# Performance work log

Hardware: AMD Instinct MI355X
Metric: run time of the kernel (lower is better)

Reference implementation:

```python
import jax, jax.numpy as jnp
import numpy as np

D = 64          # embed_dim == latent dim
T = 200         # diffusion_steps, timestep_respacing='' -> full 200 reverse steps
B, L = 8192, 100
N_ITEMS = 100000


def setup_inputs() -> dict:
    key = jax.random.key(0)
    ks = jax.random.split(key, 16)

    def lin(k, i, o):
        return (jax.random.normal(k, (i, o), jnp.float32) / np.sqrt(i)).astype(jnp.float32)

    item_seq = jax.random.randint(ks[0], (B, L), 0, N_ITEMS)
    item_emb = jax.random.normal(ks[1], (N_ITEMS, D), jnp.float32) * 0.02
    item_emb = item_emb.at[0].set(0.0)  # padding_idx=0
    return {
        'item_seq': item_seq,
        'item_emb': item_emb,
        'W_enc1': lin(ks[2], D, 256), 'b_enc1': jnp.zeros((256,), jnp.float32),
        'W_enc2': lin(ks[3], 256, 2 * D), 'b_enc2': jnp.zeros((2 * D,), jnp.float32),
        'W_in': lin(ks[4], D, D), 'b_in': jnp.zeros((D,), jnp.float32),
        'W_t': lin(ks[5], D, D), 'b_t': jnp.zeros((D,), jnp.float32),
        'W_c': lin(ks[6], D, D), 'b_c': jnp.zeros((D,), jnp.float32),
        'W_out': lin(ks[7], D, D), 'b_out': jnp.zeros((D,), jnp.float32),
    }


def _schedule():
    # improved-diffusion linear schedule
    scale = 1000.0 / T
    betas = jnp.linspace(scale * 1e-4, scale * 0.02, T, dtype=jnp.float32)
    alphas = 1.0 - betas
    acp = jnp.cumprod(alphas)
    acp_prev = jnp.concatenate([jnp.ones((1,), jnp.float32), acp[:-1]])
    sqrt_recip = jnp.sqrt(1.0 / acp)
    sqrt_recipm1 = jnp.sqrt(1.0 / acp - 1.0)
    post_var = betas * (1.0 - acp_prev) / (1.0 - acp)
    post_logvar = jnp.log(jnp.concatenate([post_var[1:2], post_var[1:]]))  # clipped
    coef1 = betas * jnp.sqrt(acp_prev) / (1.0 - acp)
    coef2 = (1.0 - acp_prev) * jnp.sqrt(alphas) / (1.0 - acp)
    return sqrt_recip, sqrt_recipm1, post_logvar, coef1, coef2


def reference(item_seq, item_emb, W_enc1, b_enc1, W_enc2, b_enc2,
              W_in, b_in, W_t, b_t, W_c, b_c, W_out, b_out):
    # ---- pooled VAE encoder (eval mode: dropout = identity, z = mu) ----
    seq = item_emb[item_seq]                                   # [B, L, D] gather
    cnt = jnp.sum(item_seq != 0, axis=1, keepdims=True).astype(seq.dtype)
    pooled = jnp.sum(seq, axis=1) / jnp.sqrt(cnt)              # [B, D]
    h = jax.nn.relu(pooled @ W_enc1 + b_enc1)
    enc = h @ W_enc2 + b_enc2                                  # [B, 2D]
    mu, logvar = jnp.split(enc, 2, axis=-1)
    z = mu                                                     # eval reparameterize

    # ---- ScoreNet: eps-prediction MLP conditioned on x_start and sinusoidal t ----
    half = D // 2
    freqs = jnp.exp(-jnp.log(10000.0) * jnp.arange(half, dtype=jnp.float32) / half)

    def scorenet(x, t_float, cond):
        ang = t_float * freqs                                  # [D/2]
        temb = jnp.concatenate([jnp.cos(ang), jnp.sin(ang)])   # [D]
        hh = jax.nn.silu(x @ W_in + b_in + (temb @ W_t + b_t) + cond @ W_c + b_c)
        return hh @ W_out + b_out                              # eps, [B, D]

    # ---- p_sample_loop (FIXED_SMALL variance, clip_denoised=True) ----
    sqrt_recip, sqrt_recipm1, post_logvar, coef1, coef2 = _schedule()
    x_init = jax.random.normal(jax.random.key(1), z.shape, z.dtype)
    noise_key = jax.random.key(2)

    def step(x, t):
        eps = scorenet(x, t.astype(jnp.float32), z)
        x0 = jnp.clip(sqrt_recip[t] * x - sqrt_recipm1[t] * eps, -1.0, 1.0)
        mean = coef1[t] * x0 + coef2[t] * x
        noise = jax.random.normal(jax.random.fold_in(noise_key, t), x.shape, x.dtype)
        sigma = jnp.where(t > 0, jnp.exp(0.5 * post_logvar[t]), 0.0)
        return mean + sigma * noise, None

    sample, _ = jax.lax.scan(step, x_init, jnp.arange(T - 1, -1, -1))
    return sample
```

## Files before the change

### kernel.cpp

```cpp
#include <hip/hip_runtime.h>
#include <cstdint>


#define DEVI __device__ __forceinline__

typedef __attribute__((ext_vector_type(8))) short short8;
typedef __attribute__((ext_vector_type(4))) float f32x4;

DEVI void threefry2x32(uint32_t k0, uint32_t k1, uint32_t x0, uint32_t x1,
                       uint32_t &o0, uint32_t &o1)
{
  const uint32_t ks2 = k0 ^ k1 ^ 0x1BD11BDAu;
  x0 += k0; x1 += k1;
#define TFR(r) { x0 += x1; x1 = __builtin_rotateleft32(x1, r); x1 ^= x0; }
  TFR(13u) TFR(15u) TFR(26u) TFR(6u)   x0 += k1;  x1 += ks2 + 1u;
  TFR(17u) TFR(29u) TFR(16u) TFR(24u)  x0 += ks2; x1 += k0 + 2u;
  TFR(13u) TFR(15u) TFR(26u) TFR(6u)   x0 += k0;  x1 += k1 + 3u;
  TFR(17u) TFR(29u) TFR(16u) TFR(24u)  x0 += k1;  x1 += ks2 + 4u;
  TFR(13u) TFR(15u) TFR(26u) TFR(6u)   x0 += ks2; x1 += k0 + 5u;
#undef TFR
  o0 = x0; o1 = x1;
}

DEVI uint32_t jax_random_bits32(uint32_t k0, uint32_t k1, uint32_t j)
{
  uint32_t a, b;
  threefry2x32(k0, k1, 0u, j, a, b);
  return a ^ b;
}

DEVI float jax_bits_to_normal(uint32_t bits)
{
  const float LO = -0.99999994f;
  float f = __uint_as_float((bits >> 9) | 0x3f800000u) - 1.0f;
  float u = fmaxf(LO, f * 2.0f + LO);
  float w = -__logf((1.0f - u) * (1.0f + u));
  float p;
  if (w < 5.0f) {
    w = w - 2.5f;
    p =              2.81022636e-08f;
    p = fmaf(p, w,   3.43273939e-07f);
    p = fmaf(p, w,  -3.5233877e-06f);
    p = fmaf(p, w,  -4.39150654e-06f);
    p = fmaf(p, w,   0.00021858087f);
    p = fmaf(p, w,  -0.00125372503f);
    p = fmaf(p, w,  -0.00417768164f);
    p = fmaf(p, w,   0.246640727f);
    p = fmaf(p, w,   1.50140941f);
  } else {
    w = sqrtf(w) - 3.0f;
    p =             -0.000200214257f;
    p = fmaf(p, w,   0.000100950558f);
    p = fmaf(p, w,   0.00134934322f);
    p = fmaf(p, w,  -0.00367342844f);
    p = fmaf(p, w,   0.00573950773f);
    p = fmaf(p, w,  -0.0076224613f);
    p = fmaf(p, w,   0.00943887047f);
    p = fmaf(p, w,   1.00167406f);
    p = fmaf(p, w,   2.83297682f);
  }
  return 1.41421356237f * (p * u);
}

DEVI short bf16_hi_trunc(float x) { return (short)(__float_as_uint(x) >> 16); }
DEVI float bf16_to_f32(short h)
{
  return __uint_as_float(((uint32_t)(unsigned short)h) << 16);
}
DEVI void split_bf16(float x, short &h, short &l)
{
  h = bf16_hi_trunc(x);
  float r = x - bf16_to_f32(h);
  l = bf16_hi_trunc(r);
}

DEVI short8 ld_frag16(const short* p)
{
  union { int4 v; short8 s; } u;
  u.v = *(const int4*)p;
  return u.s;
}

__global__ __launch_bounds__(256)
void k_pool(const int* __restrict__ seq, const float* __restrict__ emb,
            float* __restrict__ pooled)
{
  const int lane = threadIdx.x & 63;
  const int r    = blockIdx.x * 4 + (threadIdx.x >> 6);
  const int* row = seq + r * 100;
  float s = 0.f;
  int cnt = 0;
  for (int l = 0; l < 100; ++l) {
    int id = row[l];
    cnt += (id != 0);
    s += emb[id * 64 + lane];
  }
  pooled[r * 64 + lane] = s / sqrtf((float)cnt);
}

__global__ __launch_bounds__(256)
void k_enc(const float* __restrict__ pooled,
           const float* __restrict__ W1, const float* __restrict__ b1,
           const float* __restrict__ W2, const float* __restrict__ b2,
           const float* __restrict__ Wc, const float* __restrict__ bc,
           float* __restrict__ cproj)
{
  __shared__ float p_s[8][64];
  __shared__ float h_s[8][256];
  __shared__ float mu_s[8][64];
  const int tid = threadIdx.x;
  const int r0  = blockIdx.x * 8;

  for (int i = tid; i < 8 * 64; i += 256)
    p_s[i >> 6][i & 63] = pooled[r0 * 64 + i];
  __syncthreads();

  float hacc[8];
#pragma unroll
  for (int r = 0; r < 8; ++r) hacc[r] = b1[tid];
  for (int k = 0; k < 64; ++k) {
    float w = W1[k * 256 + tid];
#pragma unroll
    for (int r = 0; r < 8; ++r) hacc[r] = fmaf(p_s[r][k], w, hacc[r]);
  }
#pragma unroll
  for (int r = 0; r < 8; ++r) h_s[r][tid] = fmaxf(hacc[r], 0.f);
  __syncthreads();

#pragma unroll
  for (int pass = 0; pass < 2; ++pass) {
    int r = pass * 4 + (tid >> 6);
    int j = tid & 63;
    float acc = b2[j];
    for (int k = 0; k < 256; ++k)
      acc = fmaf(h_s[r][k], W2[k * 128 + j], acc);
    mu_s[r][j] = acc;
  }
  __syncthreads();

#pragma unroll
  for (int pass = 0; pass < 2; ++pass) {
    int r = pass * 4 + (tid >> 6);
    int j = tid & 63;
    float acc = bc[j];
    for (int k = 0; k < 64; ++k)
      acc = fmaf(mu_s[r][k], Wc[k * 64 + j], acc);
    cproj[(r0 + r) * 64 + j] = acc;
  }
}

__global__ __launch_bounds__(64)
void k_prep(const float* __restrict__ Wt, const float* __restrict__ bt,
            const float* __restrict__ bin, float* __restrict__ tpb,
            float* __restrict__ sched)
{
  __shared__ float temb[64];
  const int t = blockIdx.x;
  const int d = threadIdx.x;
  const float lg = logf(10000.0f);
  {
    int i = d & 31;
    float fr  = expf((-lg * (float)i) / 32.0f);
    float ang = (float)t * fr;
    temb[d] = (d < 32) ? cosf(ang) : sinf(ang);
  }
  if (d == 0) {
    const float start = (float)(5.0 * 1e-4);
    const float stop  = (float)(5.0 * 0.02);
    const float delta = stop - start;
    float prod = 1.f, acp_prev = 1.f, beta = 0.f, alpha = 1.f;
    for (int i = 0; i <= t; ++i) {
      beta  = start + ((float)i * delta) / 199.0f;
      alpha = 1.0f - beta;
      acp_prev = prod;
      prod = prod * alpha;
    }
    float acp = prod;
    float om  = 1.0f - acp;
    sched[t * 8 + 0] = sqrtf(1.0f / acp);
    sched[t * 8 + 1] = sqrtf(1.0f / acp - 1.0f);
    sched[t * 8 + 2] = beta * sqrtf(acp_prev) / om;
    sched[t * 8 + 3] = (1.0f - acp_prev) * sqrtf(alpha) / om;
    float pv = beta * (1.0f - acp_prev) / om;
    sched[t * 8 + 4] = (t > 0) ? sqrtf(pv) : 0.0f;
    uint32_t fk0, fk1;
    threefry2x32(0u, 2u, 0u, (uint32_t)t, fk0, fk1);
    ((uint32_t*)sched)[t * 8 + 5] = fk0;
    ((uint32_t*)sched)[t * 8 + 6] = fk1;
  }
  __syncthreads();
  float acc = bt[d] + bin[d];
  for (int k = 0; k < 64; ++k)
    acc = fmaf(temb[k], Wt[k * 64 + d], acc);
  tpb[t * 64 + d] = acc;
}

#define XLDW  72

__global__
__attribute__((amdgpu_flat_work_group_size(512, 512), amdgpu_waves_per_eu(4, 4)))
void k_ddpm(const float* __restrict__ Win, const float* __restrict__ Wout,
            const float* __restrict__ bout,
            const float* __restrict__ cproj, const float* __restrict__ tpb,
            const float* __restrict__ sched, float* __restrict__ out)
{
  __shared__ __align__(16) short Xh[16 * XLDW], Xl[16 * XLDW];
  __shared__ __align__(16) short Hh[16 * XLDW], Hl[16 * XLDW];

  const int tid  = threadIdx.x;
  const int lane = tid & 63;
  const int w    = tid >> 6;
  const int nt   = w & 3;
  const int kc   = w >> 2;
  const int nn   = lane & 15;
  const int quad = lane >> 4;
  const int dim  = nt * 16 + nn;
  const int arow = nn;
  const int r0g  = blockIdx.x * 16;
  const int kq0  = quad * 8;
  const int kq1  = 32 + quad * 8;
  const int rA   = quad * 4 + 2 * kc;

  short8 wiH0, wiL0, wiH1, wiL1, woH0, woL0, woH1, woL1;
#pragma unroll
  for (int j = 0; j < 8; ++j) {
    short h, l;
    split_bf16(Win[(kq0 + j) * 64 + dim], h, l);  wiH0[j] = h; wiL0[j] = l;
    split_bf16(Win[(kq1 + j) * 64 + dim], h, l);  wiH1[j] = h; wiL1[j] = l;
    split_bf16(Wout[(kq0 + j) * 64 + dim], h, l); woH0[j] = h; woL0[j] = l;
    split_bf16(Wout[(kq1 + j) * 64 + dim], h, l); woH1[j] = h; woL1[j] = l;
  }

  const float bo = bout[dim];
  const uint32_t jA = (uint32_t)((r0g + rA) * 64 + dim);
  const uint32_t jB = jA + 64u;
  const float cpA = cproj[jA];
  const float cpB = cproj[jB];

  float xoA = jax_bits_to_normal(jax_random_bits32(0u, 1u, jA));
  float xoB = jax_bits_to_normal(jax_random_bits32(0u, 1u, jB));
  {
    short h, l;
    split_bf16(xoA, h, l); Xh[rA * XLDW + dim] = h; Xl[rA * XLDW + dim] = l;
    split_bf16(xoB, h, l); Xh[(rA+1) * XLDW + dim] = h; Xl[(rA+1) * XLDW + dim] = l;
  }
  __syncthreads();

  float tp = tpb[199 * 64 + dim];

#pragma unroll 1
  for (int t = 199; t >= 0; --t) {
    const float sr   = sched[t * 8 + 0];
    const float srm1 = sched[t * 8 + 1];
    const float c1   = sched[t * 8 + 2];
    const float c2   = sched[t * 8 + 3];
    const float sg   = sched[t * 8 + 4];
    const uint32_t fk0 = ((const uint32_t*)sched)[t * 8 + 5];
    const uint32_t fk1 = ((const uint32_t*)sched)[t * 8 + 6];

    float nA = jax_bits_to_normal(jax_random_bits32(fk0, fk1, jA));
    float nB = jax_bits_to_normal(jax_random_bits32(fk0, fk1, jB));

    f32x4 acc;
    if (kc == 0) { acc[0] = tp + cpA; acc[1] = tp + cpB; acc[2] = 0.f; acc[3] = 0.f; }
    else         { acc[0] = 0.f; acc[1] = 0.f; acc[2] = tp + cpA; acc[3] = tp + cpB; }
    {
      short8 xh0 = ld_frag16(&Xh[arow * XLDW + kq0]);
      short8 xl0 = ld_frag16(&Xl[arow * XLDW + kq0]);
      short8 xh1 = ld_frag16(&Xh[arow * XLDW + kq1]);
      short8 xl1 = ld_frag16(&Xl[arow * XLDW + kq1]);
      acc = __builtin_amdgcn_mfma_f32_16x16x32_bf16(xl0, wiH0, acc, 0, 0, 0);
      acc = __builtin_amdgcn_mfma_f32_16x16x32_bf16(xh0, wiL0, acc, 0, 0, 0);
      acc = __builtin_amdgcn_mfma_f32_16x16x32_bf16(xh0, wiH0, acc, 0, 0, 0);
      acc = __builtin_amdgcn_mfma_f32_16x16x32_bf16(xl1, wiH1, acc, 0, 0, 0);
      acc = __builtin_amdgcn_mfma_f32_16x16x32_bf16(xh1, wiL1, acc, 0, 0, 0);
      acc = __builtin_amdgcn_mfma_f32_16x16x32_bf16(xh1, wiH1, acc, 0, 0, 0);
    }
    {
      float vA, vB;
      if (kc == 0) { vA = acc[0]; vB = acc[1]; }
      else         { vA = acc[2]; vB = acc[3]; }
      vA = vA * __builtin_amdgcn_rcpf(1.0f + __expf(-vA));
      vB = vB * __builtin_amdgcn_rcpf(1.0f + __expf(-vB));
      short h, l;
      split_bf16(vA, h, l); Hh[rA * XLDW + dim] = h; Hl[rA * XLDW + dim] = l;
      split_bf16(vB, h, l); Hh[(rA+1) * XLDW + dim] = h; Hl[(rA+1) * XLDW + dim] = l;
    }
    int tn = (t > 0) ? (t - 1) : 0;
    float tpn = tpb[tn * 64 + dim];
    __syncthreads();

    f32x4 eac;
    if (kc == 0) { eac[0] = bo; eac[1] = bo; eac[2] = 0.f; eac[3] = 0.f; }
    else         { eac[0] = 0.f; eac[1] = 0.f; eac[2] = bo; eac[3] = bo; }
    {
      short8 hh0 = ld_frag16(&Hh[arow * XLDW + kq0]);
      short8 hl0 = ld_frag16(&Hl[arow * XLDW + kq0]);
      short8 hh1 = ld_frag16(&Hh[arow * XLDW + kq1]);
      short8 hl1 = ld_frag16(&Hl[arow * XLDW + kq1]);
      eac = __builtin_amdgcn_mfma_f32_16x16x32_bf16(hl0, woH0, eac, 0, 0, 0);
      eac = __builtin_amdgcn_mfma_f32_16x16x32_bf16(hh0, woL0, eac, 0, 0, 0);
      eac = __builtin_amdgcn_mfma_f32_16x16x32_bf16(hh0, woH0, eac, 0, 0, 0);
      eac = __builtin_amdgcn_mfma_f32_16x16x32_bf16(hl1, woH1, eac, 0, 0, 0);
      eac = __builtin_amdgcn_mfma_f32_16x16x32_bf16(hh1, woL1, eac, 0, 0, 0);
      eac = __builtin_amdgcn_mfma_f32_16x16x32_bf16(hh1, woH1, eac, 0, 0, 0);
    }
    {
      float eA, eB;
      if (kc == 0) { eA = eac[0]; eB = eac[1]; }
      else         { eA = eac[2]; eB = eac[3]; }
      float xcA = fminf(1.f, fmaxf(-1.f, sr * xoA - srm1 * eA));
      float xcB = fminf(1.f, fmaxf(-1.f, sr * xoB - srm1 * eB));
      xoA = c1 * xcA + c2 * xoA + sg * nA;
      xoB = c1 * xcB + c2 * xoB + sg * nB;
      short h, l;
      split_bf16(xoA, h, l); Xh[rA * XLDW + dim] = h; Xl[rA * XLDW + dim] = l;
      split_bf16(xoB, h, l); Xh[(rA+1) * XLDW + dim] = h; Xl[(rA+1) * XLDW + dim] = l;
      tp = tpn;
    }
    __syncthreads();
  }

  out[jA] = xoA;
  out[jB] = xoB;
}

extern "C" void kernel_launch(void* const* d_in, const int* in_sizes, int n_in,
                              void* d_out, int out_size, void* d_ws, size_t ws_size,
                              hipStream_t stream)
{
  const int*   seq  = (const int*)  d_in[0];
  const float* emb  = (const float*)d_in[1];
  const float* W1   = (const float*)d_in[2];
  const float* b1   = (const float*)d_in[3];
  const float* W2   = (const float*)d_in[4];
  const float* b2   = (const float*)d_in[5];
  const float* Win  = (const float*)d_in[6];
  const float* bin  = (const float*)d_in[7];
  const float* Wt   = (const float*)d_in[8];
  const float* bt   = (const float*)d_in[9];
  const float* Wc   = (const float*)d_in[10];
  const float* bc   = (const float*)d_in[11];
  const float* Wout = (const float*)d_in[12];
  const float* bout = (const float*)d_in[13];

  float* out   = (float*)d_out;
  float* ws    = (float*)d_ws;
  float* cproj = ws;
  float* tpb   = ws + 524288;
  float* sched = ws + 524288 + 12800;
  float* pooled = out;

  k_pool <<<2048, 256, 0, stream>>>(seq, emb, pooled);
  k_enc  <<<1024, 256, 0, stream>>>(pooled, W1, b1, W2, b2, Wc, bc, cproj);
  k_prep <<<200, 64, 0, stream>>>(Wt, bt, bin, tpb, sched);
  k_ddpm <<<512, 512, 0, stream>>>(Win, Wout, bout, cproj, tpb, sched, out);
}
```

Baseline: 561.4 us.

## Precompute all diffusion noise in a parallel kernel before the sampling loop

Adds a k_noise kernel that generates the threefry-based Gaussian noise for all 200 timesteps into a large workspace buffer. The serial k_ddpm loop then loads each step's noise from memory instead of computing the RNG inline. This takes the integer hash work off the latency-bound sequential loop and runs it in a fully parallel launch. In exchange it writes and later reads about 400 MB of noise. It is only enabled when the workspace is large enough, otherwise the old inline path is used.

```diff
diff --git a/kernel.cpp b/kernel.cpp
--- a/kernel.cpp
+++ b/kernel.cpp
@@ -195,14 +195,32 @@
   tpb[t * 64 + d] = acc;
 }
 
+__global__ __launch_bounds__(256)
+void k_noise(const float* __restrict__ sched, float* __restrict__ noise)
+{
+  const uint32_t base = (blockIdx.x * 256u + threadIdx.x) * 4u;
+  const uint32_t t = base >> 19;
+  const uint32_t j = base & 524287u;
+  const uint32_t fk0 = ((const uint32_t*)sched)[t * 8 + 5];
+  const uint32_t fk1 = ((const uint32_t*)sched)[t * 8 + 6];
+  float4 v;
+  v.x = jax_bits_to_normal(jax_random_bits32(fk0, fk1, j + 0u));
+  v.y = jax_bits_to_normal(jax_random_bits32(fk0, fk1, j + 1u));
+  v.z = jax_bits_to_normal(jax_random_bits32(fk0, fk1, j + 2u));
+  v.w = jax_bits_to_normal(jax_random_bits32(fk0, fk1, j + 3u));
+  *(float4*)(noise + base) = v;
+}
+
 #define XLDW  72
 
+template <bool PRE>
 __global__
 __attribute__((amdgpu_flat_work_group_size(512, 512), amdgpu_waves_per_eu(4, 4)))
 void k_ddpm(const float* __restrict__ Win, const float* __restrict__ Wout,
             const float* __restrict__ bout,
             const float* __restrict__ cproj, const float* __restrict__ tpb,
-            const float* __restrict__ sched, float* __restrict__ out)
+            const float* __restrict__ sched, const float* __restrict__ noise,
+            float* __restrict__ out)
 {
   __shared__ __align__(16) short Xh[16 * XLDW], Xl[16 * XLDW];
   __shared__ __align__(16) short Hh[16 * XLDW], Hl[16 * XLDW];
@@ -255,11 +273,18 @@
     const float c1   = sched[t * 8 + 2];
     const float c2   = sched[t * 8 + 3];
     const float sg   = sched[t * 8 + 4];
-    const uint32_t fk0 = ((const uint32_t*)sched)[t * 8 + 5];
-    const uint32_t fk1 = ((const uint32_t*)sched)[t * 8 + 6];
-
-    float nA = jax_bits_to_normal(jax_random_bits32(fk0, fk1, jA));
-    float nB = jax_bits_to_normal(jax_random_bits32(fk0, fk1, jB));
+
+    float nA, nB;
+    if (PRE) {
+      const float* np = noise + (uint32_t)t * 524288u;
+      nA = np[jA];
+      nB = np[jB];
+    } else {
+      const uint32_t fk0 = ((const uint32_t*)sched)[t * 8 + 5];
+      const uint32_t fk1 = ((const uint32_t*)sched)[t * 8 + 6];
+      nA = jax_bits_to_normal(jax_random_bits32(fk0, fk1, jA));
+      nB = jax_bits_to_normal(jax_random_bits32(fk0, fk1, jB));
+    }
 
     f32x4 acc;
     if (kc == 0) { acc[0] = tp + cpA; acc[1] = tp + cpB; acc[2] = 0.f; acc[3] = 0.f; }
@@ -349,10 +374,18 @@
   float* cproj = ws;
   float* tpb   = ws + 524288;
   float* sched = ws + 524288 + 12800;
+  float* noise = ws + 538688;
   float* pooled = out;
+
+  const bool pre = ws_size >= (538688ull + 104857600ull) * 4ull;
 
   k_pool <<<2048, 256, 0, stream>>>(seq, emb, pooled);
   k_enc  <<<1024, 256, 0, stream>>>(pooled, W1, b1, W2, b2, Wc, bc, cproj);
   k_prep <<<200, 64, 0, stream>>>(Wt, bt, bin, tpb, sched);
-  k_ddpm <<<512, 512, 0, stream>>>(Win, Wout, bout, cproj, tpb, sched, out);
-}
+  if (pre) {
+    k_noise<<<102400, 256, 0, stream>>>(sched, noise);
+    k_ddpm<true> <<<512, 512, 0, stream>>>(Win, Wout, bout, cproj, tpb, sched, noise, out);
+  } else {
+    k_ddpm<false><<<512, 512, 0, stream>>>(Win, Wout, bout, cproj, tpb, sched, noise, out);
+  }
+}
```

New measurement: 562.4 us. No clear change (+0.2%).

## Specialize warps: four do GEMV steps, four pre-generate next-step noise

Applied to the files above, without the earlier changes.

Splits the 8 waves of each block into two roles. Four waves do the two MFMA GEMVs and the update for all 16 rows, each covering all four accumulator rows. The other four waves compute next-step threefry normal noise into a double-buffered shared-memory buffer. This takes the RNG cost off the critical path of the sequential diffusion loop, but it removes the old split-K duplication, so the GEMV waves now do four rows each and half the waves are producers.

```diff
diff --git a/kernel.cpp b/kernel.cpp
--- a/kernel.cpp
+++ b/kernel.cpp
@@ -196,6 +196,7 @@
 }
 
 #define XLDW  72
+#define NBW   68
 
 __global__
 __attribute__((amdgpu_flat_work_group_size(512, 512), amdgpu_waves_per_eu(4, 4)))
@@ -206,123 +207,155 @@
 {
   __shared__ __align__(16) short Xh[16 * XLDW], Xl[16 * XLDW];
   __shared__ __align__(16) short Hh[16 * XLDW], Hl[16 * XLDW];
+  __shared__ __align__(16) float nbuf[2 * 16 * NBW];
 
   const int tid  = threadIdx.x;
   const int lane = tid & 63;
   const int w    = tid >> 6;
+  const bool gemv = (w < 4);
+  const int r0g  = blockIdx.x * 16;
+  const uint32_t* su = (const uint32_t*)sched;
+
   const int nt   = w & 3;
-  const int kc   = w >> 2;
   const int nn   = lane & 15;
   const int quad = lane >> 4;
   const int dim  = nt * 16 + nn;
   const int arow = nn;
-  const int r0g  = blockIdx.x * 16;
   const int kq0  = quad * 8;
   const int kq1  = 32 + quad * 8;
-  const int rA   = quad * 4 + 2 * kc;
+  const int rowb = quad * 4;
+
+  const int q    = (w - 4) * 64 + lane;
+  const int cb   = q * 4;
+  const uint32_t jn = (uint32_t)(r0g * 64 + cb);
+  const int nrow = cb >> 6;
+  const int ndim = cb & 63;
+  float* nb_w = &nbuf[nrow * NBW + ndim];
 
   short8 wiH0, wiL0, wiH1, wiL1, woH0, woL0, woH1, woL1;
-#pragma unroll
-  for (int j = 0; j < 8; ++j) {
-    short h, l;
-    split_bf16(Win[(kq0 + j) * 64 + dim], h, l);  wiH0[j] = h; wiL0[j] = l;
-    split_bf16(Win[(kq1 + j) * 64 + dim], h, l);  wiH1[j] = h; wiL1[j] = l;
-    split_bf16(Wout[(kq0 + j) * 64 + dim], h, l); woH0[j] = h; woL0[j] = l;
-    split_bf16(Wout[(kq1 + j) * 64 + dim], h, l); woH1[j] = h; woL1[j] = l;
-  }
-
-  const float bo = bout[dim];
-  const uint32_t jA = (uint32_t)((r0g + rA) * 64 + dim);
-  const uint32_t jB = jA + 64u;
-  const float cpA = cproj[jA];
-  const float cpB = cproj[jB];
-
-  float xoA = jax_bits_to_normal(jax_random_bits32(0u, 1u, jA));
-  float xoB = jax_bits_to_normal(jax_random_bits32(0u, 1u, jB));
-  {
-    short h, l;
-    split_bf16(xoA, h, l); Xh[rA * XLDW + dim] = h; Xl[rA * XLDW + dim] = l;
-    split_bf16(xoB, h, l); Xh[(rA+1) * XLDW + dim] = h; Xl[(rA+1) * XLDW + dim] = l;
-  }
-  __syncthreads();
-
-  float tp = tpb[199 * 64 + dim];
+  float cp[4], xo[4];
+  float bo = 0.f, tp = 0.f;
+  uint32_t j0 = 0;
+
+  if (gemv) {
+#pragma unroll
+    for (int j = 0; j < 8; ++j) {
+      short h, l;
+      split_bf16(Win[(kq0 + j) * 64 + dim], h, l);  wiH0[j] = h; wiL0[j] = l;
+      split_bf16(Win[(kq1 + j) * 64 + dim], h, l);  wiH1[j] = h; wiL1[j] = l;
+      split_bf16(Wout[(kq0 + j) * 64 + dim], h, l); woH0[j] = h; woL0[j] = l;
+      split_bf16(Wout[(kq1 + j) * 64 + dim], h, l); woH1[j] = h; woL1[j] = l;
+    }
+    bo = bout[dim];
+    j0 = (uint32_t)((r0g + rowb) * 64 + dim);
+#pragma unroll
+    for (int r = 0; r < 4; ++r) cp[r] = cproj[j0 + r * 64u];
+#pragma unroll
+    for (int r = 0; r < 4; ++r) {
+      xo[r] = jax_bits_to_normal(jax_random_bits32(0u, 1u, j0 + r * 64u));
+      short h, l;
+      split_bf16(xo[r], h, l);
+      Xh[(rowb + r) * XLDW + dim] = h; Xl[(rowb + r) * XLDW + dim] = l;
+    }
+    tp = tpb[199 * 64 + dim];
+  } else {
+    const uint32_t fk0 = su[199 * 8 + 5];
+    const uint32_t fk1 = su[199 * 8 + 6];
+    float* d = nb_w + 16 * NBW;
+    d[0] = jax_bits_to_normal(jax_random_bits32(fk0, fk1, jn + 0u));
+    d[1] = jax_bits_to_normal(jax_random_bits32(fk0, fk1, jn + 1u));
+    d[2] = jax_bits_to_normal(jax_random_bits32(fk0, fk1, jn + 2u));
+    d[3] = jax_bits_to_normal(jax_random_bits32(fk0, fk1, jn + 3u));
+  }
+  __syncthreads();
 
 #pragma unroll 1
   for (int t = 199; t >= 0; --t) {
-    const float sr   = sched[t * 8 + 0];
-    const float srm1 = sched[t * 8 + 1];
-    const float c1   = sched[t * 8 + 2];
-    const float c2   = sched[t * 8 + 3];
-    const float sg   = sched[t * 8 + 4];
-    const uint32_t fk0 = ((const uint32_t*)sched)[t * 8 + 5];
-    const uint32_t fk1 = ((const uint32_t*)sched)[t * 8 + 6];
-
-    float nA = jax_bits_to_normal(jax_random_bits32(fk0, fk1, jA));
-    float nB = jax_bits_to_normal(jax_random_bits32(fk0, fk1, jB));
-
+    float sr = 0.f, srm1 = 0.f, c1 = 0.f, c2 = 0.f, sg = 0.f;
+    float n[4], tpn = 0.f;
     f32x4 acc;
-    if (kc == 0) { acc[0] = tp + cpA; acc[1] = tp + cpB; acc[2] = 0.f; acc[3] = 0.f; }
-    else         { acc[0] = 0.f; acc[1] = 0.f; acc[2] = tp + cpA; acc[3] = tp + cpB; }
-    {
-      short8 xh0 = ld_frag16(&Xh[arow * XLDW + kq0]);
-      short8 xl0 = ld_frag16(&Xl[arow * XLDW + kq0]);
-      short8 xh1 = ld_frag16(&Xh[arow * XLDW + kq1]);
-      short8 xl1 = ld_frag16(&Xl[arow * XLDW + kq1]);
-      acc = __builtin_amdgcn_mfma_f32_16x16x32_bf16(xl0, wiH0, acc, 0, 0, 0);
-      acc = __builtin_amdgcn_mfma_f32_16x16x32_bf16(xh0, wiL0, acc, 0, 0, 0);
-      acc = __builtin_amdgcn_mfma_f32_16x16x32_bf16(xh0, wiH0, acc, 0, 0, 0);
-      acc = __builtin_amdgcn_mfma_f32_16x16x32_bf16(xl1, wiH1, acc, 0, 0, 0);
-      acc = __builtin_amdgcn_mfma_f32_16x16x32_bf16(xh1, wiL1, acc, 0, 0, 0);
-      acc = __builtin_amdgcn_mfma_f32_16x16x32_bf16(xh1, wiH1, acc, 0, 0, 0);
-    }
-    {
-      float vA, vB;
-      if (kc == 0) { vA = acc[0]; vB = acc[1]; }
-      else         { vA = acc[2]; vB = acc[3]; }
-      vA = vA * __builtin_amdgcn_rcpf(1.0f + __expf(-vA));
-      vB = vB * __builtin_amdgcn_rcpf(1.0f + __expf(-vB));
-      short h, l;
-      split_bf16(vA, h, l); Hh[rA * XLDW + dim] = h; Hl[rA * XLDW + dim] = l;
-      split_bf16(vB, h, l); Hh[(rA+1) * XLDW + dim] = h; Hl[(rA+1) * XLDW + dim] = l;
-    }
-    int tn = (t > 0) ? (t - 1) : 0;
-    float tpn = tpb[tn * 64 + dim];
+    uint32_t gk0 = 0, gk1 = 0;
+    float* nd = nullptr;
+
+    if (gemv) {
+      sr   = sched[t * 8 + 0];
+      srm1 = sched[t * 8 + 1];
+      c1   = sched[t * 8 + 2];
+      c2   = sched[t * 8 + 3];
+      sg   = sched[t * 8 + 4];
+      const float* nr = &nbuf[(t & 1) * 16 * NBW + rowb * NBW + dim];
+#pragma unroll
+      for (int r = 0; r < 4; ++r) n[r] = nr[r * NBW];
+
+#pragma unroll
+      for (int r = 0; r < 4; ++r) acc[r] = tp + cp[r];
+      {
+        short8 xh0 = ld_frag16(&Xh[arow * XLDW + kq0]);
+        short8 xl0 = ld_frag16(&Xl[arow * XLDW + kq0]);
+        short8 xh1 = ld_frag16(&Xh[arow * XLDW + kq1]);
+        short8 xl1 = ld_frag16(&Xl[arow * XLDW + kq1]);
+        acc = __builtin_amdgcn_mfma_f32_16x16x32_bf16(xl0, wiH0, acc, 0, 0, 0);
+        acc = __builtin_amdgcn_mfma_f32_16x16x32_bf16(xh0, wiL0, acc, 0, 0, 0);
+        acc = __builtin_amdgcn_mfma_f32_16x16x32_bf16(xh0, wiH0, acc, 0, 0, 0);
+        acc = __builtin_amdgcn_mfma_f32_16x16x32_bf16(xl1, wiH1, acc, 0, 0, 0);
+        acc = __builtin_amdgcn_mfma_f32_16x16x32_bf16(xh1, wiL1, acc, 0, 0, 0);
+        acc = __builtin_amdgcn_mfma_f32_16x16x32_bf16(xh1, wiH1, acc, 0, 0, 0);
+      }
+#pragma unroll
+      for (int r = 0; r < 4; ++r) {
+        float v = acc[r];
+        v = v * __builtin_amdgcn_rcpf(1.0f + __expf(-v));
+        short h, l;
+        split_bf16(v, h, l);
+        Hh[(rowb + r) * XLDW + dim] = h; Hl[(rowb + r) * XLDW + dim] = l;
+      }
+      int tn = (t > 0) ? (t - 1) : 0;
+      tpn = tpb[tn * 64 + dim];
+    } else if (t > 0) {
+      gk0 = su[(t - 1) * 8 + 5];
+      gk1 = su[(t - 1) * 8 + 6];
+      nd = nb_w + ((t - 1) & 1) * 16 * NBW;
+      nd[0] = jax_bits_to_normal(jax_random_bits32(gk0, gk1, jn + 0u));
+      nd[1] = jax_bits_to_normal(jax_random_bits32(gk0, gk1, jn + 1u));
+    }
     __syncthreads();
 
-    f32x4 eac;
-    if (kc == 0) { eac[0] = bo; eac[1] = bo; eac[2] = 0.f; eac[3] = 0.f; }
-    else         { eac[0] = 0.f; eac[1] = 0.f; eac[2] = bo; eac[3] = bo; }
-    {
-      short8 hh0 = ld_frag16(&Hh[arow * XLDW + kq0]);
-      short8 hl0 = ld_frag16(&Hl[arow * XLDW + kq0]);
-      short8 hh1 = ld_frag16(&Hh[arow * XLDW + kq1]);
-      short8 hl1 = ld_frag16(&Hl[arow * XLDW + kq1]);
-      eac = __builtin_amdgcn_mfma_f32_16x16x32_bf16(hl0, woH0, eac, 0, 0, 0);
-      eac = __builtin_amdgcn_mfma_f32_16x16x32_bf16(hh0, woL0, eac, 0, 0, 0);
-      eac = __builtin_amdgcn_mfma_f32_16x16x32_bf16(hh0, woH0, eac, 0, 0, 0);
-      eac = __builtin_amdgcn_mfma_f32_16x16x32_bf16(hl1, woH1, eac, 0, 0, 0);
-      eac = __builtin_amdgcn_mfma_f32_16x16x32_bf16(hh1, woL1, eac, 0, 0, 0);
-      eac = __builtin_amdgcn_mfma_f32_16x16x32_bf16(hh1, woH1, eac, 0, 0, 0);
-    }
-    {
-      float eA, eB;
-      if (kc == 0) { eA = eac[0]; eB = eac[1]; }
-      else         { eA = eac[2]; eB = eac[3]; }
-      float xcA = fminf(1.f, fmaxf(-1.f, sr * xoA - srm1 * eA));
-      float xcB = fminf(1.f, fmaxf(-1.f, sr * xoB - srm1 * eB));
-      xoA = c1 * xcA + c2 * xoA + sg * nA;
-      xoB = c1 * xcB + c2 * xoB + sg * nB;
-      short h, l;
-      split_bf16(xoA, h, l); Xh[rA * XLDW + dim] = h; Xl[rA * XLDW + dim] = l;
-      split_bf16(xoB, h, l); Xh[(rA+1) * XLDW + dim] = h; Xl[(rA+1) * XLDW + dim] = l;
+    if (gemv) {
+      f32x4 eac;
+#pragma unroll
+      for (int r = 0; r < 4; ++r) eac[r] = bo;
+      {
+        short8 hh0 = ld_frag16(&Hh[arow * XLDW + kq0]);
+        short8 hl0 = ld_frag16(&Hl[arow * XLDW + kq0]);
+        short8 hh1 = ld_frag16(&Hh[arow * XLDW + kq1]);
+        short8 hl1 = ld_frag16(&Hl[arow * XLDW + kq1]);
+        eac = __builtin_amdgcn_mfma_f32_16x16x32_bf16(hl0, woH0, eac, 0, 0, 0);
+        eac = __builtin_amdgcn_mfma_f32_16x16x32_bf16(hh0, woL0, eac, 0, 0, 0);
+        eac = __builtin_amdgcn_mfma_f32_16x16x32_bf16(hh0, woH0, eac, 0, 0, 0);
+        eac = __builtin_amdgcn_mfma_f32_16x16x32_bf16(hl1, woH1, eac, 0, 0, 0);
+        eac = __builtin_amdgcn_mfma_f32_16x16x32_bf16(hh1, woL1, eac, 0, 0, 0);
+        eac = __builtin_amdgcn_mfma_f32_16x16x32_bf16(hh1, woH1, eac, 0, 0, 0);
+      }
+#pragma unroll
+      for (int r = 0; r < 4; ++r) {
+        float xc = fminf(1.f, fmaxf(-1.f, sr * xo[r] - srm1 * eac[r]));
+        xo[r] = c1 * xc + c2 * xo[r] + sg * n[r];
+        short h, l;
+        split_bf16(xo[r], h, l);
+        Xh[(rowb + r) * XLDW + dim] = h; Xl[(rowb + r) * XLDW + dim] = l;
+      }
       tp = tpn;
+    } else if (t > 0) {
+      nd[2] = jax_bits_to_normal(jax_random_bits32(gk0, gk1, jn + 2u));
+      nd[3] = jax_bits_to_normal(jax_random_bits32(gk0, gk1, jn + 3u));
     }
     __syncthreads();
   }
 
-  out[jA] = xoA;
-  out[jB] = xoB;
+  if (gemv) {
+#pragma unroll
+    for (int r = 0; r < 4; ++r) out[j0 + r * 64u] = xo[r];
+  }
 }
 
 extern "C" void kernel_launch(void* const* d_in, const int* in_sizes, int n_in,
```

Result: faster. 543.5 us (-3.2%).
